# Kernel tuning notes

Measured on AMD Instinct MI355X. Metric: run time of the kernel, lower is better.

## Reference

```python
import jax, jax.numpy as jnp
import numpy as np

EPS = 1e-3  # keras LayerNormalization default epsilon


def setup_inputs() -> dict:
    key = jax.random.key(0)
    ks = jax.random.split(key, 6)
    B, T, D, U = 128, 512, 512, 512
    scale = 1.0 / np.sqrt(U + D)
    return {
        "x": jax.random.normal(ks[0], (B, T, D), jnp.float32),
        "h0": jnp.zeros((B, U), jnp.float32),
        "c0": jnp.zeros((B, U), jnp.float32),
        "Wf": jax.random.normal(ks[1], (U, U + D), jnp.float32) * scale,
        "bf": jnp.zeros((U,), jnp.float32),
        "Wg": jax.random.normal(ks[2], (U, U + D), jnp.float32) * scale,
        "bg": jnp.zeros((U,), jnp.float32),
        "Wi": jax.random.normal(ks[3], (U, U + D), jnp.float32) * scale,
        "bi": jnp.zeros((U,), jnp.float32),
        "Wo": jax.random.normal(ks[4], (U, U + D), jnp.float32) * scale,
        "bo": jnp.zeros((U,), jnp.float32),
        "gamma": jnp.ones((U,), jnp.float32),
        "beta": jnp.zeros((U,), jnp.float32),
    }


def reference(x, h0, c0, Wf, bf, Wg, bg, Wi, bi, Wo, bo, gamma, beta):
    # Stack the 4 gate weights/biases: one GEMM per step instead of four.
    W = jnp.stack([Wf, Wg, Wi, Wo])          # [4, U, U+D]
    b = jnp.stack([bf, bg, bi, bo])          # [4, U]

    def ln(z):
        # shared LayerNormalization over the last (units) axis
        m = jnp.mean(z, axis=-1, keepdims=True)
        v = jnp.var(z, axis=-1, keepdims=True)
        return (z - m) * jax.lax.rsqrt(v + EPS) * gamma + beta

    def step(carry, xt):
        h, c = carry                          # [B, U] each
        cat = jnp.concatenate([h, xt], axis=-1)   # [B, U+D]
        z = jnp.einsum('bd,gud->bgu', cat, W) + b  # [B, 4, U]
        z = ln(z)                             # LN per gate over units
        f = jax.nn.sigmoid(z[:, 0])
        g = jnp.tanh(z[:, 1])
        i = jax.nn.sigmoid(z[:, 2])
        o = jax.nn.sigmoid(z[:, 3])
        c_new = c * f + g * i
        c_ln = ln(c_new)                      # layer_norm_c_state: carried c is normalized
        h_new = o * jnp.tanh(c_ln)
        return (h_new, c_ln), h_new

    xs = jnp.swapaxes(x, 0, 1)                # [T, B, D]
    (_, _), hs = jax.lax.scan(step, (h0, c0), xs)
    return jnp.swapaxes(hs, 0, 1)             # [B, T, U]
```

## Files before the change

### kernel.cpp

```cpp
#include <hip/hip_runtime.h>
#include <hip/hip_fp16.h>


typedef unsigned short ushort_t;
typedef unsigned long long u64;
typedef __attribute__((ext_vector_type(8))) short short8;
typedef __attribute__((ext_vector_type(4))) float f32x4;

#define Bsz 128
#define Tn  512
#define Un  512
#define NU  2048
#define NC  16
#define WPC 16
#define BPC 8

__device__ __forceinline__ ushort_t f2bf(float f){
  unsigned u = __float_as_uint(f);
  u = u + 0x7fffu + ((u >> 16) & 1u);
  return (ushort_t)(u >> 16);
}
__device__ __forceinline__ float bf2f(ushort_t h){
  return __uint_as_float(((unsigned)h) << 16);
}
__device__ __forceinline__ float sigf(float x){
  float e = __expf(-x);
  return __builtin_amdgcn_rcpf(1.0f + e);
}
__device__ __forceinline__ float tanh_fast(float x){
  float ax = fabsf(x);
  float e  = __expf(-2.0f*ax);
  float r  = (1.0f - e) * __builtin_amdgcn_rcpf(1.0f + e);
  return x >= 0.0f ? r : -r;
}

__device__ __forceinline__ void st_tag(u64* p, float v, unsigned tag){
  u64 w = ((u64)tag << 32) | (u64)__float_as_uint(v);
  __hip_atomic_store(p, w, __ATOMIC_RELAXED, __HIP_MEMORY_SCOPE_AGENT);
}
__device__ __forceinline__ void st_f32(float* p, float v){
  __hip_atomic_store(p, v, __ATOMIC_RELAXED, __HIP_MEMORY_SCOPE_AGENT);
}
__device__ __forceinline__ u64 ld_u64(const u64* p){
  return __hip_atomic_load(p, __ATOMIC_RELAXED, __HIP_MEMORY_SCOPE_AGENT);
}
__device__ __forceinline__ float lo_f(u64 w){ return __uint_as_float((unsigned)w); }
__device__ __forceinline__ float hi_f(u64 w){ return __uint_as_float((unsigned)(w >> 32)); }

__global__ void k_prep_w(const float* __restrict__ Wf, const float* __restrict__ Wg,
                         const float* __restrict__ Wi, const float* __restrict__ Wo,
                         ushort_t* __restrict__ wh_hi, ushort_t* __restrict__ wh_lo){
  int idx = blockIdx.x*blockDim.x + threadIdx.x;
  if (idx >= 1048576) return;
  const float* Wp[4] = {Wf, Wg, Wi, Wo};
  int j = idx & 7;
  int lane = (idx >> 3) & 63;
  int i = (idx >> 9) & 31;
  int wslot = idx >> 14;
  int kiter = i >> 1, nt = i & 1;
  int wid = wslot >> 2, wave = wslot & 3;
  int n = wid*128 + wave*32 + nt*16 + (lane & 15);
  int k = kiter*32 + (lane >> 4)*8 + j;
  int gate = n >> 9, u = n & 511;
  float w = Wp[gate][u*1024 + k];
  ushort_t hi = f2bf(w);
  wh_hi[idx] = hi;
  wh_lo[idx] = f2bf(w - bf2f(hi));
}

__global__ __launch_bounds__(256,2) void k_gemm_xz(const float* __restrict__ A,
    const float* __restrict__ Wf, const float* __restrict__ Wg,
    const float* __restrict__ Wi, const float* __restrict__ Wo,
    __half* __restrict__ C){
  __shared__ __align__(16) ushort_t Ah[128*32];
  __shared__ __align__(16) ushort_t Al[128*32];
  __shared__ __align__(16) ushort_t Bh[128*32];
  __shared__ __align__(16) ushort_t Bl[128*32];
  const int tid  = threadIdx.x;
  const int lane = tid & 63, wave = tid >> 6;
  const int quad = lane >> 4, l15 = lane & 15;
  const int wm = wave >> 1, wn = wave & 1;
  const int m0 = blockIdx.x * 128, n0 = blockIdx.y * 128;
  const float* Wp = (n0 < 512) ? Wf : (n0 < 1024) ? Wg : (n0 < 1536) ? Wi : Wo;
  const int u0 = n0 & 511;
  f32x4 acc[4][4];
  #pragma unroll
  for (int a=0;a<4;a++)
    #pragma unroll
    for (int b=0;b<4;b++) acc[a][b] = (f32x4){0.f,0.f,0.f,0.f};

  for (int kc = 0; kc < 512; kc += 32){
    __syncthreads();
    #pragma unroll
    for (int p=0; p<4; p++){
      int slot = p*256 + tid;
      int row = slot >> 3, seg = slot & 7;
      float4 va = *(const float4*)(A  + (size_t)(m0+row)*512  + kc + seg*4);
      float4 vb = *(const float4*)(Wp + (size_t)(u0+row)*1024 + 512 + kc + seg*4);
      ushort4 ah, al, bh, bl;
      ah.x=f2bf(va.x); al.x=f2bf(va.x-bf2f(ah.x));
      ah.y=f2bf(va.y); al.y=f2bf(va.y-bf2f(ah.y));
      ah.z=f2bf(va.z); al.z=f2bf(va.z-bf2f(ah.z));
      ah.w=f2bf(va.w); al.w=f2bf(va.w-bf2f(ah.w));
      bh.x=f2bf(vb.x); bl.x=f2bf(vb.x-bf2f(bh.x));
      bh.y=f2bf(vb.y); bl.y=f2bf(vb.y-bf2f(bh.y));
      bh.z=f2bf(vb.z); bl.z=f2bf(vb.z-bf2f(bh.z));
      bh.w=f2bf(vb.w); bl.w=f2bf(vb.w-bf2f(bh.w));
      *(ushort4*)(Ah + slot*4) = ah;
      *(ushort4*)(Al + slot*4) = al;
      *(ushort4*)(Bh + slot*4) = bh;
      *(ushort4*)(Bl + slot*4) = bl;
    }
    __syncthreads();
    short8 afh[4], afl[4], bfh[4], bfl[4];
    #pragma unroll
    for (int ti=0; ti<4; ti++){
      afh[ti] = *(const short8*)(Ah + (wm*64 + ti*16 + l15)*32 + quad*8);
      afl[ti] = *(const short8*)(Al + (wm*64 + ti*16 + l15)*32 + quad*8);
    }
    #pragma unroll
    for (int tj=0; tj<4; tj++){
      bfh[tj] = *(const short8*)(Bh + (wn*64 + tj*16 + l15)*32 + quad*8);
      bfl[tj] = *(const short8*)(Bl + (wn*64 + tj*16 + l15)*32 + quad*8);
    }
    #pragma unroll
    for (int ti=0; ti<4; ti++)
      #pragma unroll
      for (int tj=0; tj<4; tj++){
        acc[ti][tj] = __builtin_amdgcn_mfma_f32_16x16x32_bf16(afh[ti], bfh[tj], acc[ti][tj], 0,0,0);
        acc[ti][tj] = __builtin_amdgcn_mfma_f32_16x16x32_bf16(afl[ti], bfh[tj], acc[ti][tj], 0,0,0);
        acc[ti][tj] = __builtin_amdgcn_mfma_f32_16x16x32_bf16(afh[ti], bfl[tj], acc[ti][tj], 0,0,0);
      }
  }
  #pragma unroll
  for (int ti=0; ti<4; ti++)
    #pragma unroll
    for (int tj=0; tj<4; tj++)
      #pragma unroll
      for (int r=0; r<4; r++){
        int m = m0 + wm*64 + ti*16 + quad*4 + r;
        int n = n0 + wn*64 + tj*16 + l15;
        C[(size_t)m*NU + n] = __float2half(acc[ti][tj][r]);
      }
}

__global__ __launch_bounds__(256,1) void k_lstm(
    const ushort_t* __restrict__ wh_hi_g, const ushort_t* __restrict__ wh_lo_g,
    const __half* __restrict__ xz,
    const float* __restrict__ bfp, const float* __restrict__ bgp,
    const float* __restrict__ bip, const float* __restrict__ bop,
    const float* __restrict__ gamma, const float* __restrict__ beta,
    const float* __restrict__ h0, const float* __restrict__ c0,
    float* __restrict__ actf, u64* __restrict__ zpart,
    u64* __restrict__ aflag,
    float* __restrict__ out)
{
  const int bid = blockIdx.x;
  const int cid = bid & 15;
  const int wid = bid >> 4;
  const int tid = threadIdx.x;
  const int wave = tid >> 6, lane = tid & 63;
  const int quad = lane >> 4, l15 = lane & 15;
  const int gate = wid >> 2;

  __shared__ __align__(16) ushort_t h_hi[16][520];
  __shared__ __align__(16) ushort_t h_lo[16][520];
  __shared__ float wavepart[4][8][2];

  for (int i = tid; i < 16*520; i += 256){
    int r = i / 520, u = i - r*520;
    float v = (r < BPC && u < 512) ? h0[(cid*BPC + r)*512 + u] : 0.0f;
    ushort_t hh = f2bf(v);
    h_hi[r][u] = hh;
    h_lo[r][u] = f2bf(v - bf2f(hh));
  }

  const int b_loc = tid >> 5;
  const int l2 = (tid & 31) << 1;
  float c[16];
  float gam16[16], bet16[16];
  #pragma unroll
  for (int i=0;i<16;i++){
    int u = (i>>1)*64 + l2 + (i&1);
    c[i] = c0[(cid*BPC + b_loc)*512 + u];
    gam16[i] = gamma[u]; bet16[i] = beta[u];
  }

  short8 wrh[32], wrl[32];
  {
    const ushort_t* wph = wh_hi_g + (size_t)(wid*4 + wave)*16384 + lane*8;
    const ushort_t* wpl = wh_lo_g + (size_t)(wid*4 + wave)*16384 + lane*8;
    #pragma unroll
    for (int i=0;i<32;i++){
      wrh[i] = *(const short8*)(wph + (size_t)i*512);
      wrl[i] = *(const short8*)(wpl + (size_t)i*512);
    }
  }

  float bias_r[2], gam_r[2], bet_r[2];
  int ng_[2];
  #pragma unroll
  for (int nt=0; nt<2; nt++){
    int ng = wid*128 + wave*32 + nt*16 + l15;
    ng_[nt] = ng;
    int u = ng & 511;
    const float* bp = (gate==0)? bfp : (gate==1)? bgp : (gate==2)? bip : bop;
    bias_r[nt] = bp[u];
    gam_r[nt] = gamma[u]; bet_r[nt] = beta[u];
  }
  const bool bvalid = (quad < 2);
  const int b_base = quad*4;

  __syncthreads();

  for (int t = 0; t < Tn; ++t){
    const unsigned tag = (unsigned)(t + 1);
    const int par = t & 1;
    const size_t fb = (size_t)(par*NC + cid)*WPC;
    float xzv[2][4];
    #pragma unroll
    for (int nt=0; nt<2; nt++)
      #pragma unroll
      for (int r=0; r<4; r++){
        if (bvalid){
          int b = cid*BPC + b_base + r;
          xzv[nt][r] = __half2float(xz[((size_t)b*Tn + t)*NU + ng_[nt]]);
        } else xzv[nt][r] = 0.0f;
      }
    f32x4 acc0 = (f32x4){0.f,0.f,0.f,0.f}, acc1 = (f32x4){0.f,0.f,0.f,0.f};
    #pragma unroll
    for (int ki=0; ki<16; ki++){
      short8 afh = *(const short8*)(&h_hi[l15][ki*32 + quad*8]);
      short8 afl = *(const short8*)(&h_lo[l15][ki*32 + quad*8]);
      acc0 = __builtin_amdgcn_mfma_f32_16x16x32_bf16(afh, wrh[2*ki+0], acc0, 0,0,0);
      acc0 = __builtin_amdgcn_mfma_f32_16x16x32_bf16(afl, wrh[2*ki+0], acc0, 0,0,0);
      acc0 = __builtin_amdgcn_mfma_f32_16x16x32_bf16(afh, wrl[2*ki+0], acc0, 0,0,0);
      acc1 = __builtin_amdgcn_mfma_f32_16x16x32_bf16(afh, wrh[2*ki+1], acc1, 0,0,0);
      acc1 = __builtin_amdgcn_mfma_f32_16x16x32_bf16(afl, wrh[2*ki+1], acc1, 0,0,0);
      acc1 = __builtin_amdgcn_mfma_f32_16x16x32_bf16(afh, wrl[2*ki+1], acc1, 0,0,0);
    }
    float z[2][4];
    #pragma unroll
    for (int r=0;r<4;r++){
      z[0][r] = bvalid ? (acc0[r] + xzv[0][r] + bias_r[0]) : 0.0f;
      z[1][r] = bvalid ? (acc1[r] + xzv[1][r] + bias_r[1]) : 0.0f;
    }
    float sum[4], ssq[4];
    #pragma unroll
    for (int r=0;r<4;r++){
      float s = z[0][r] + z[1][r];
      float q = z[0][r]*z[0][r] + z[1][r]*z[1][r];
      #pragma unroll
      for (int off=1; off<16; off<<=1){ s += __shfl_xor(s, off); q += __shfl_xor(q, off); }
      sum[r]=s; ssq[r]=q;
    }
    if (l15 == 0 && bvalid){
      #pragma unroll
      for (int r=0;r<4;r++){
        wavepart[wave][b_base + r][0] = sum[r];
        wavepart[wave][b_base + r][1] = ssq[r];
      }
    }
    __syncthreads();
    if (tid < 8){
      float S = wavepart[0][tid][0] + wavepart[1][tid][0] + wavepart[2][tid][0] + wavepart[3][tid][0];
      float Q = wavepart[0][tid][1] + wavepart[1][tid][1] + wavepart[2][tid][1] + wavepart[3][tid][1];
      u64* zp = zpart + ((fb + wid)*BPC + tid)*2;
      st_tag(zp+0, S, tag);
      st_tag(zp+1, Q, tag);
    }
    __syncthreads();

    if (bvalid){
      u64 zv[16][2];
      #pragma unroll
      for (int j=0;j<4;j++)
        #pragma unroll
        for (int r=0;r<4;r++){
          const u64* zp = zpart + ((fb + gate*4 + j)*BPC + b_base + r)*2;
          zv[j*4+r][0] = ld_u64(zp+0);
          zv[j*4+r][1] = ld_u64(zp+1);
        }
      unsigned miss;
      do {
        miss = 0u;
        #pragma unroll
        for (int j=0;j<4;j++)
          #pragma unroll
          for (int r=0;r<4;r++){
            const u64* zp = zpart + ((fb + gate*4 + j)*BPC + b_base + r)*2;
            if ((unsigned)(zv[j*4+r][0] >> 32) != tag){ zv[j*4+r][0] = ld_u64(zp+0); miss = 1u; }
            if ((unsigned)(zv[j*4+r][1] >> 32) != tag){ zv[j*4+r][1] = ld_u64(zp+1); miss = 1u; }
          }
        if (miss) __builtin_amdgcn_s_sleep(1);
      } while (miss);
      #pragma unroll
      for (int r=0;r<4;r++){
        float S = lo_f(zv[0*4+r][0]) + lo_f(zv[1*4+r][0]) + lo_f(zv[2*4+r][0]) + lo_f(zv[3*4+r][0]);
        float Q = lo_f(zv[0*4+r][1]) + lo_f(zv[1*4+r][1]) + lo_f(zv[2*4+r][1]) + lo_f(zv[3*4+r][1]);
        float m_ = S * (1.0f/512.0f);
        float var = Q * (1.0f/512.0f) - m_*m_;
        float rstd = rsqrtf(var + 1e-3f);
        #pragma unroll
        for (int nt=0;nt<2;nt++){
          float zn = (z[nt][r] - m_) * rstd * gam_r[nt] + bet_r[nt];
          float a = (gate==1) ? tanh_fast(zn) : sigf(zn);
          st_f32(actf + (size_t)((par*NC + cid)*BPC + b_base + r)*NU + ng_[nt], a);
        }
      }
    }
    asm volatile("s_waitcnt vmcnt(0)" ::: "memory");
    __syncthreads();
    if (tid == 0) st_tag(aflag + fb + wid, 0.0f, tag);
    if (tid < 16 && tid != wid){
      const u64* fp = aflag + fb + tid;
      while ((unsigned)(ld_u64(fp) >> 32) != tag) { }
    }
    __syncthreads();

    {
      const float* abf = actf + (size_t)((par*NC + cid)*BPC + b_loc)*NU;
      float cn[16], og[16];
      float ls = 0.f, lq = 0.f;
      #pragma unroll
      for (int ch=0; ch<2; ch++){
        u64 w[4][4];
        #pragma unroll
        for (int g=0; g<4; g++)
          #pragma unroll
          for (int jj=0; jj<4; jj++)
            w[g][jj] = ld_u64((const u64*)(abf + (size_t)g*512 + (ch*4+jj)*64 + l2));
        #pragma unroll
        for (int jj=0; jj<4; jj++)
          #pragma unroll
          for (int e=0; e<2; e++){
            int k = ch*8 + jj*2 + e;
            float fv = e ? hi_f(w[0][jj]) : lo_f(w[0][jj]);
            float gv = e ? hi_f(w[1][jj]) : lo_f(w[1][jj]);
            float iv = e ? hi_f(w[2][jj]) : lo_f(w[2][jj]);
            float ov = e ? hi_f(w[3][jj]) : lo_f(w[3][jj]);
            float cv = c[k]*fv + gv*iv;
            cn[k] = cv;
            og[k] = ov;
            ls += cv; lq += cv*cv;
          }
      }
      #pragma unroll
      for (int off=1; off<32; off<<=1){ ls += __shfl_xor(ls, off); lq += __shfl_xor(lq, off); }
      float m_ = ls*(1.0f/512.0f);
      float var = lq*(1.0f/512.0f) - m_*m_;
      float rs = rsqrtf(var + 1e-3f);
      #pragma unroll
      for (int j=0; j<8; j++){
        int u0 = j*64 + l2;
        float cl0 = (cn[2*j+0]-m_)*rs*gam16[2*j+0] + bet16[2*j+0];
        float cl1 = (cn[2*j+1]-m_)*rs*gam16[2*j+1] + bet16[2*j+1];
        c[2*j+0] = cl0; c[2*j+1] = cl1;
        float hv0 = og[2*j+0]*tanh_fast(cl0);
        float hv1 = og[2*j+1]*tanh_fast(cl1);
        ushort2 hh; hh.x = f2bf(hv0); hh.y = f2bf(hv1);
        ushort2 hl; hl.x = f2bf(hv0 - bf2f(hh.x)); hl.y = f2bf(hv1 - bf2f(hh.y));
        *(ushort2*)&h_hi[b_loc][u0] = hh;
        *(ushort2*)&h_lo[b_loc][u0] = hl;
        if (wid == 0){
          float2 hv; hv.x = hv0; hv.y = hv1;
          *(float2*)&out[((size_t)(cid*BPC + b_loc)*Tn + t)*Un + u0] = hv;
        }
      }
    }
    __syncthreads();
  }
}

extern "C" void kernel_launch(void* const* d_in, const int* in_sizes, int n_in,
                              void* d_out, int out_size, void* d_ws, size_t ws_size,
                              hipStream_t stream){
  const float* x     = (const float*)d_in[0];
  const float* h0    = (const float*)d_in[1];
  const float* c0    = (const float*)d_in[2];
  const float* Wf    = (const float*)d_in[3];
  const float* bf_   = (const float*)d_in[4];
  const float* Wg    = (const float*)d_in[5];
  const float* bg_   = (const float*)d_in[6];
  const float* Wi    = (const float*)d_in[7];
  const float* bi_   = (const float*)d_in[8];
  const float* Wo    = (const float*)d_in[9];
  const float* bo_   = (const float*)d_in[10];
  const float* gamma = (const float*)d_in[11];
  const float* beta  = (const float*)d_in[12];

  char* ws = (char*)d_ws;
  __half*   xz    = (__half*)(ws);
  ushort_t* wh_hi = (ushort_t*)(ws + (256ull<<20));
  ushort_t* wh_lo = (ushort_t*)(ws + (258ull<<20));
  float*    actf  = (float*)(ws + (260ull<<20));
  u64*      zpart = (u64*)(ws + (262ull<<20));
  u64*      aflag = (u64*)(ws + (262ull<<20) + (64ull<<10));
  float* out = (float*)d_out;

  hipMemsetAsync(zpart, 0, (64ull<<10) + (4ull<<10), stream);
  k_prep_w<<<4096, 256, 0, stream>>>(Wf, Wg, Wi, Wo, wh_hi, wh_lo);
  dim3 g(Bsz*Tn/128, NU/128);
  k_gemm_xz<<<g, 256, 0, stream>>>(x, Wf, Wg, Wi, Wo, xz);
  k_lstm<<<256, 256, 0, stream>>>(wh_hi, wh_lo, xz, bf_, bg_, bi_, bo_, gamma, beta, h0, c0,
                                  actf, zpart, aflag, out);
}
```

Before: 6.435 ms.

## Replace per-step flag barrier with tagged activation words and local partial reuse

```diff
diff --git a/kernel.cpp b/kernel.cpp
--- a/kernel.cpp
+++ b/kernel.cpp
@@ -15,6 +15,10 @@
 #define WPC 16
 #define BPC 8
 
+#define BARRIER() do{ asm volatile("s_waitcnt lgkmcnt(0)" ::: "memory"); \
+  __builtin_amdgcn_sched_barrier(0); __builtin_amdgcn_s_barrier(); \
+  asm volatile("" ::: "memory"); }while(0)
+
 __device__ __forceinline__ ushort_t f2bf(float f){
   unsigned u = __float_as_uint(f);
   u = u + 0x7fffu + ((u >> 16) & 1u);
@@ -38,14 +42,13 @@
   u64 w = ((u64)tag << 32) | (u64)__float_as_uint(v);
   __hip_atomic_store(p, w, __ATOMIC_RELAXED, __HIP_MEMORY_SCOPE_AGENT);
 }
-__device__ __forceinline__ void st_f32(float* p, float v){
-  __hip_atomic_store(p, v, __ATOMIC_RELAXED, __HIP_MEMORY_SCOPE_AGENT);
+__device__ __forceinline__ void st_u64(u64* p, u64 w){
+  __hip_atomic_store(p, w, __ATOMIC_RELAXED, __HIP_MEMORY_SCOPE_AGENT);
 }
 __device__ __forceinline__ u64 ld_u64(const u64* p){
   return __hip_atomic_load(p, __ATOMIC_RELAXED, __HIP_MEMORY_SCOPE_AGENT);
 }
 __device__ __forceinline__ float lo_f(u64 w){ return __uint_as_float((unsigned)w); }
-__device__ __forceinline__ float hi_f(u64 w){ return __uint_as_float((unsigned)(w >> 32)); }
 
 __global__ void k_prep_w(const float* __restrict__ Wf, const float* __restrict__ Wg,
                          const float* __restrict__ Wi, const float* __restrict__ Wo,
@@ -151,8 +154,7 @@
     const float* __restrict__ bip, const float* __restrict__ bop,
     const float* __restrict__ gamma, const float* __restrict__ beta,
     const float* __restrict__ h0, const float* __restrict__ c0,
-    float* __restrict__ actf, u64* __restrict__ zpart,
-    u64* __restrict__ aflag,
+    u64* __restrict__ actw, u64* __restrict__ zpart,
     float* __restrict__ out)
 {
   const int bid = blockIdx.x;
@@ -162,6 +164,7 @@
   const int wave = tid >> 6, lane = tid & 63;
   const int quad = lane >> 4, l15 = lane & 15;
   const int gate = wid >> 2;
+  const int j_own = wid & 3;
 
   __shared__ __align__(16) ushort_t h_hi[16][520];
   __shared__ __align__(16) ushort_t h_lo[16][520];
@@ -176,14 +179,14 @@
   }
 
   const int b_loc = tid >> 5;
-  const int l2 = (tid & 31) << 1;
-  float c[16];
-  float gam16[16], bet16[16];
+  const int l5 = tid & 31;
+  const int q5 = l5 >> 4, s5 = l5 & 15;
+  float c[16], gam16[16], bet16[16];
   #pragma unroll
-  for (int i=0;i<16;i++){
-    int u = (i>>1)*64 + l2 + (i&1);
-    c[i] = c0[(cid*BPC + b_loc)*512 + u];
-    gam16[i] = gamma[u]; bet16[i] = beta[u];
+  for (int k=0;k<16;k++){
+    int u = (k>>1)*64 + q5*32 + (k&1)*16 + s5;
+    c[k] = c0[(cid*BPC + b_loc)*512 + u];
+    gam16[k] = gamma[u]; bet16[k] = beta[u];
   }
 
   short8 wrh[32], wrl[32];
@@ -210,13 +213,17 @@
   }
   const bool bvalid = (quad < 2);
   const int b_base = quad*4;
+  const int wrd = ((wid & 3)*4 + wave)*16 + l15;
 
   __syncthreads();
 
   for (int t = 0; t < Tn; ++t){
     const unsigned tag = (unsigned)(t + 1);
+    const unsigned tag8 = (unsigned)((t + 1) & 0xFF);
     const int par = t & 1;
-    const size_t fb = (size_t)(par*NC + cid)*WPC;
+    const size_t fbz  = (size_t)(par*NC + cid)*WPC;
+    const size_t arow = (size_t)(par*NC + cid)*BPC;
+
     float xzv[2][4];
     #pragma unroll
     for (int nt=0; nt<2; nt++)
@@ -249,10 +256,10 @@
     #pragma unroll
     for (int r=0;r<4;r++){
       float s = z[0][r] + z[1][r];
-      float q = z[0][r]*z[0][r] + z[1][r]*z[1][r];
-      #pragma unroll
-      for (int off=1; off<16; off<<=1){ s += __shfl_xor(s, off); q += __shfl_xor(q, off); }
-      sum[r]=s; ssq[r]=q;
+      float qq = z[0][r]*z[0][r] + z[1][r]*z[1][r];
+      #pragma unroll
+      for (int off=1; off<16; off<<=1){ s += __shfl_xor(s, off); qq += __shfl_xor(qq, off); }
+      sum[r]=s; ssq[r]=qq;
     }
     if (l15 == 0 && bvalid){
       #pragma unroll
@@ -261,84 +268,98 @@
         wavepart[wave][b_base + r][1] = ssq[r];
       }
     }
-    __syncthreads();
+    BARRIER();
     if (tid < 8){
       float S = wavepart[0][tid][0] + wavepart[1][tid][0] + wavepart[2][tid][0] + wavepart[3][tid][0];
       float Q = wavepart[0][tid][1] + wavepart[1][tid][1] + wavepart[2][tid][1] + wavepart[3][tid][1];
-      u64* zp = zpart + ((fb + wid)*BPC + tid)*2;
+      u64* zp = zpart + ((fbz + wid)*BPC + tid)*2;
       st_tag(zp+0, S, tag);
       st_tag(zp+1, Q, tag);
     }
-    __syncthreads();
 
     if (bvalid){
-      u64 zv[16][2];
-      #pragma unroll
-      for (int j=0;j<4;j++)
+      u64 zv[4][4][2];
+      #pragma unroll
+      for (int j=0;j<4;j++) if (j != j_own)
         #pragma unroll
         for (int r=0;r<4;r++){
-          const u64* zp = zpart + ((fb + gate*4 + j)*BPC + b_base + r)*2;
-          zv[j*4+r][0] = ld_u64(zp+0);
-          zv[j*4+r][1] = ld_u64(zp+1);
+          const u64* zp = zpart + ((fbz + gate*4 + j)*BPC + b_base + r)*2;
+          zv[j][r][0] = ld_u64(zp+0);
+          zv[j][r][1] = ld_u64(zp+1);
         }
       unsigned miss;
       do {
         miss = 0u;
         #pragma unroll
-        for (int j=0;j<4;j++)
+        for (int j=0;j<4;j++) if (j != j_own)
           #pragma unroll
           for (int r=0;r<4;r++){
-            const u64* zp = zpart + ((fb + gate*4 + j)*BPC + b_base + r)*2;
-            if ((unsigned)(zv[j*4+r][0] >> 32) != tag){ zv[j*4+r][0] = ld_u64(zp+0); miss = 1u; }
-            if ((unsigned)(zv[j*4+r][1] >> 32) != tag){ zv[j*4+r][1] = ld_u64(zp+1); miss = 1u; }
+            const u64* zp = zpart + ((fbz + gate*4 + j)*BPC + b_base + r)*2;
+            if ((unsigned)(zv[j][r][0] >> 32) != tag){ zv[j][r][0] = ld_u64(zp+0); miss = 1u; }
+            if ((unsigned)(zv[j][r][1] >> 32) != tag){ zv[j][r][1] = ld_u64(zp+1); miss = 1u; }
           }
-        if (miss) __builtin_amdgcn_s_sleep(1);
+        if (miss) __builtin_amdgcn_s_sleep(2);
       } while (miss);
       #pragma unroll
       for (int r=0;r<4;r++){
-        float S = lo_f(zv[0*4+r][0]) + lo_f(zv[1*4+r][0]) + lo_f(zv[2*4+r][0]) + lo_f(zv[3*4+r][0]);
-        float Q = lo_f(zv[0*4+r][1]) + lo_f(zv[1*4+r][1]) + lo_f(zv[2*4+r][1]) + lo_f(zv[3*4+r][1]);
+        float S = wavepart[0][b_base+r][0] + wavepart[1][b_base+r][0]
+                + wavepart[2][b_base+r][0] + wavepart[3][b_base+r][0];
+        float Q = wavepart[0][b_base+r][1] + wavepart[1][b_base+r][1]
+                + wavepart[2][b_base+r][1] + wavepart[3][b_base+r][1];
+        #pragma unroll
+        for (int j=0;j<4;j++) if (j != j_own){ S += lo_f(zv[j][r][0]); Q += lo_f(zv[j][r][1]); }
         float m_ = S * (1.0f/512.0f);
         float var = Q * (1.0f/512.0f) - m_*m_;
         float rstd = rsqrtf(var + 1e-3f);
-        #pragma unroll
-        for (int nt=0;nt<2;nt++){
-          float zn = (z[nt][r] - m_) * rstd * gam_r[nt] + bet_r[nt];
-          float a = (gate==1) ? tanh_fast(zn) : sigf(zn);
-          st_f32(actf + (size_t)((par*NC + cid)*BPC + b_base + r)*NU + ng_[nt], a);
-        }
-      }
-    }
-    asm volatile("s_waitcnt vmcnt(0)" ::: "memory");
-    __syncthreads();
-    if (tid == 0) st_tag(aflag + fb + wid, 0.0f, tag);
-    if (tid < 16 && tid != wid){
-      const u64* fp = aflag + fb + tid;
-      while ((unsigned)(ld_u64(fp) >> 32) != tag) { }
-    }
-    __syncthreads();
+        float zn0 = (z[0][r] - m_) * rstd * gam_r[0] + bet_r[0];
+        float zn1 = (z[1][r] - m_) * rstd * gam_r[1] + bet_r[1];
+        float a0 = (gate==1) ? tanh_fast(zn0) : sigf(zn0);
+        float a1 = (gate==1) ? tanh_fast(zn1) : sigf(zn1);
+        unsigned p0 = (__float_as_uint(a0) & 0xFFFFFF00u) | tag8;
+        unsigned p1 = (__float_as_uint(a1) & 0xFFFFFF00u) | tag8;
+        st_u64(actw + (arow + b_base + r)*1024 + gate*256 + wrd,
+               ((u64)p1 << 32) | (u64)p0);
+      }
+    }
 
     {
-      const float* abf = actf + (size_t)((par*NC + cid)*BPC + b_loc)*NU;
+      const u64* ab = actw + (arow + b_loc)*1024;
+      if (!bvalid) __builtin_amdgcn_s_sleep(32);
       float cn[16], og[16];
       float ls = 0.f, lq = 0.f;
       #pragma unroll
       for (int ch=0; ch<2; ch++){
-        u64 w[4][4];
+        u64 aw[4][4];
         #pragma unroll
         for (int g=0; g<4; g++)
           #pragma unroll
           for (int jj=0; jj<4; jj++)
-            w[g][jj] = ld_u64((const u64*)(abf + (size_t)g*512 + (ch*4+jj)*64 + l2));
+            aw[g][jj] = ld_u64(ab + g*256 + (ch*4+jj)*32 + l5);
+        unsigned amiss;
+        do {
+          amiss = 0u;
+          #pragma unroll
+          for (int g=0; g<4; g++)
+            #pragma unroll
+            for (int jj=0; jj<4; jj++)
+              if ((unsigned)(aw[g][jj] & 0xFF) != tag8){
+                aw[g][jj] = ld_u64(ab + g*256 + (ch*4+jj)*32 + l5); amiss = 1u;
+              }
+          if (amiss) __builtin_amdgcn_s_sleep(8);
+        } while (amiss);
         #pragma unroll
         for (int jj=0; jj<4; jj++)
           #pragma unroll
           for (int e=0; e<2; e++){
-            int k = ch*8 + jj*2 + e;
-            float fv = e ? hi_f(w[0][jj]) : lo_f(w[0][jj]);
-            float gv = e ? hi_f(w[1][jj]) : lo_f(w[1][jj]);
-            float iv = e ? hi_f(w[2][jj]) : lo_f(w[2][jj]);
-            float ov = e ? hi_f(w[3][jj]) : lo_f(w[3][jj]);
+            int k = (ch*4+jj)*2 + e;
+            unsigned bf = e ? (unsigned)(aw[0][jj] >> 32) : (unsigned)aw[0][jj];
+            unsigned bg = e ? (unsigned)(aw[1][jj] >> 32) : (unsigned)aw[1][jj];
+            unsigned bi = e ? (unsigned)(aw[2][jj] >> 32) : (unsigned)aw[2][jj];
+            unsigned bo = e ? (unsigned)(aw[3][jj] >> 32) : (unsigned)aw[3][jj];
+            float fv = __uint_as_float(bf & 0xFFFFFF00u);
+            float gv = __uint_as_float(bg & 0xFFFFFF00u);
+            float iv = __uint_as_float(bi & 0xFFFFFF00u);
+            float ov = __uint_as_float(bo & 0xFFFFFF00u);
             float cv = c[k]*fv + gv*iv;
             cn[k] = cv;
             og[k] = ov;
@@ -351,24 +372,18 @@
       float var = lq*(1.0f/512.0f) - m_*m_;
       float rs = rsqrtf(var + 1e-3f);
       #pragma unroll
-      for (int j=0; j<8; j++){
-        int u0 = j*64 + l2;
-        float cl0 = (cn[2*j+0]-m_)*rs*gam16[2*j+0] + bet16[2*j+0];
-        float cl1 = (cn[2*j+1]-m_)*rs*gam16[2*j+1] + bet16[2*j+1];
-        c[2*j+0] = cl0; c[2*j+1] = cl1;
-        float hv0 = og[2*j+0]*tanh_fast(cl0);
-        float hv1 = og[2*j+1]*tanh_fast(cl1);
-        ushort2 hh; hh.x = f2bf(hv0); hh.y = f2bf(hv1);
-        ushort2 hl; hl.x = f2bf(hv0 - bf2f(hh.x)); hl.y = f2bf(hv1 - bf2f(hh.y));
-        *(ushort2*)&h_hi[b_loc][u0] = hh;
-        *(ushort2*)&h_lo[b_loc][u0] = hl;
-        if (wid == 0){
-          float2 hv; hv.x = hv0; hv.y = hv1;
-          *(float2*)&out[((size_t)(cid*BPC + b_loc)*Tn + t)*Un + u0] = hv;
-        }
-      }
-    }
-    __syncthreads();
+      for (int k=0; k<16; k++){
+        int u = (k>>1)*64 + q5*32 + (k&1)*16 + s5;
+        float cl = (cn[k]-m_)*rs*gam16[k] + bet16[k];
+        c[k] = cl;
+        float hv = og[k]*tanh_fast(cl);
+        ushort_t hh = f2bf(hv);
+        h_hi[b_loc][u] = hh;
+        h_lo[b_loc][u] = f2bf(hv - bf2f(hh));
+        if (wid == 0) out[((size_t)(cid*BPC + b_loc)*Tn + t)*Un + u] = hv;
+      }
+    }
+    BARRIER();
   }
 }
 
@@ -393,15 +408,14 @@
   __half*   xz    = (__half*)(ws);
   ushort_t* wh_hi = (ushort_t*)(ws + (256ull<<20));
   ushort_t* wh_lo = (ushort_t*)(ws + (258ull<<20));
-  float*    actf  = (float*)(ws + (260ull<<20));
+  u64*      actw  = (u64*)(ws + (260ull<<20));
   u64*      zpart = (u64*)(ws + (262ull<<20));
-  u64*      aflag = (u64*)(ws + (262ull<<20) + (64ull<<10));
   float* out = (float*)d_out;
 
-  hipMemsetAsync(zpart, 0, (64ull<<10) + (4ull<<10), stream);
+  hipMemsetAsync(actw, 0, (2ull<<20) + (64ull<<10), stream);
   k_prep_w<<<4096, 256, 0, stream>>>(Wf, Wg, Wi, Wo, wh_hi, wh_lo);
   dim3 g(Bsz*Tn/128, NU/128);
   k_gemm_xz<<<g, 256, 0, stream>>>(x, Wf, Wg, Wi, Wo, xz);
   k_lstm<<<256, 256, 0, stream>>>(wh_hi, wh_lo, xz, bf_, bg_, bi_, bo_, gamma, beta, h0, c0,
-                                  actf, zpart, aflag, out);
-}
+                                  actw, zpart, out);
+}
```

New measurement: 6.557 ms. About the same (+1.9%).
